# Kernel tuning notes

Measured on AMD Instinct MI355X. Metric: run time of the kernel, lower is better.

## Reference

```python
import jax, jax.numpy as jnp
import numpy as np

SHRINK_THRES = 0.0025
R_THRES = 1.0
EPS = 1e-12


def setup_inputs() -> dict:
    key = jax.random.key(0)
    k1, k2 = jax.random.split(key)
    N, L, D = 16384, 4096, 1024  # samples, memory slots (lan_dim), fea_dim
    x = jax.random.normal(k1, (N, D), dtype=jnp.float32)
    stdv = 1.0 / np.sqrt(D)
    weight = jax.random.uniform(k2, (L, D), dtype=jnp.float32, minval=-stdv, maxval=stdv)
    return {"x": x, "weight": weight}


def reference(x, weight):
    # memory addressing: att = softmax(x @ W^T)  -> [N, L]
    att = jax.nn.softmax(x @ weight.T, axis=1)
    # hard_shrink_relu: relu(a - lambd) * a / (|a - lambd| + eps)
    shifted = att - SHRINK_THRES
    att = jax.nn.relu(shifted) * att / (jnp.abs(shifted) + EPS)
    # L1 normalize along dim 1 (F.normalize p=1, eps=1e-12)
    l1 = jnp.sum(jnp.abs(att), axis=1, keepdims=True)
    att = att / jnp.maximum(l1, EPS)
    # reconstruct from memory: [N, D]
    output = att @ weight
    # nearest landmark per sample (detached gather in original)
    ind = jnp.argmax(att, axis=1)                      # [N]
    nl = weight[ind]                                   # [N, D]
    # second-nearest: overwrite argmax slot with the row minimum, re-argmax
    rows = jnp.arange(att.shape[0])
    row_min = jnp.min(att, axis=1)
    att2 = att.at[rows, ind].set(row_min)
    ind2 = jnp.argmax(att2, axis=1)
    nl2 = weight[ind2]                                 # [N, D]
    # centroid-distance filter (original returns list of indices; we return a
    # jit-compatible boolean mask over samples instead)
    cen = jnp.mean(weight, axis=0)                     # [D]
    dist = jnp.sqrt(jnp.sum((x - cen) ** 2, axis=1))   # [N]
    col_mask = dist < R_THRES                          # [N] bool
    return (output, att, nl, nl2, col_mask)
```

## Files before the change

### kernel.cpp

```cpp
#include <hip/hip_runtime.h>
#include <cmath>

#define NS 16384
#define LS 4096
#define DF 1024
#define SHRINK_T 0.0025f
#define EPS_T 1e-12f

using f16 = _Float16;
using f16x4 = __attribute__((ext_vector_type(4))) _Float16;
using f16x8 = __attribute__((ext_vector_type(8))) _Float16;
using f32x4 = __attribute__((ext_vector_type(4))) float;

__global__ void split_kernel(const float* __restrict__ src,
                             f16* __restrict__ hi, f16* __restrict__ lo, int n4) {
    int i = blockIdx.x * 256 + threadIdx.x;
    if (i >= n4) return;
    float4 v = reinterpret_cast<const float4*>(src)[i];
    f16x4 h, l;
    h[0] = (f16)v.x; h[1] = (f16)v.y; h[2] = (f16)v.z; h[3] = (f16)v.w;
    l[0] = (f16)(v.x - (float)h[0]);
    l[1] = (f16)(v.y - (float)h[1]);
    l[2] = (f16)(v.z - (float)h[2]);
    l[3] = (f16)(v.w - (float)h[3]);
    reinterpret_cast<f16x4*>(hi)[i] = h;
    reinterpret_cast<f16x4*>(lo)[i] = l;
}

__global__ void centroid_kernel(const float* __restrict__ w, float* __restrict__ cen) {
    int c = blockIdx.x * 256 + threadIdx.x;
    if (c >= DF) return;
    float acc = 0.f;
    for (int l = 0; l < LS; ++l) acc += w[(size_t)l * DF + c];
    cen[c] = acc * (1.0f / (float)LS);
}

#define BM 128
#define BN 128
#define BK 32

#define GLOAD16(gptr, lptr)                                                    \
    __builtin_amdgcn_global_load_lds(                                          \
        (const __attribute__((address_space(1))) void*)(gptr),                 \
        (__attribute__((address_space(3))) void*)(lptr), 16, 0, 0)

__global__ __launch_bounds__(256) void gemm_f16_kernel(
    const f16* __restrict__ xh, const f16* __restrict__ xl,
    const f16* __restrict__ wh, const f16* __restrict__ wl,
    float* __restrict__ S, int r0, int rowsChunk)
{
    __shared__ __align__(16) f16 Ah[BM * BK];
    __shared__ __align__(16) f16 Al[BM * BK];
    __shared__ __align__(16) f16 Bh[BN * BK];
    __shared__ __align__(16) f16 Bl[BN * BK];

    const int t = threadIdx.x;
    const int lane = t & 63;
    const int wv = t >> 6;
    const int wr = (wv >> 1) * 64;
    const int wc = (wv & 1) * 64;
    const int rowBase = r0 + blockIdx.y * BM;
    const int colBase = blockIdx.x * BN;

    f32x4 acc[4][4];
#pragma unroll
    for (int m = 0; m < 4; ++m)
#pragma unroll
        for (int n = 0; n < 4; ++n)
            acc[m][n] = (f32x4){0.f, 0.f, 0.f, 0.f};

    const int fr = lane & 15;
    const int fq = lane >> 4;
    const int kq = fq * 8;

    for (int k0 = 0; k0 < DF; k0 += BK) {
#pragma unroll
        for (int h = 0; h < 2; ++h) {
            const int sr = h * 64 + (t >> 2);
            const int cc = (t & 3) * 8;
            int ga = rowBase + sr; if (ga >= NS) ga = NS - 1;
            const int gb = colBase + sr;
            const int lbase = (h * 64 + wv * 16) * BK;
            GLOAD16(xh + (size_t)ga * DF + k0 + cc, &Ah[lbase]);
            GLOAD16(xl + (size_t)ga * DF + k0 + cc, &Al[lbase]);
            GLOAD16(wh + (size_t)gb * DF + k0 + cc, &Bh[lbase]);
            GLOAD16(wl + (size_t)gb * DF + k0 + cc, &Bl[lbase]);
        }
        __syncthreads();

        f16x8 amh[4], aml[4], bnh[4], bnl[4];
#pragma unroll
        for (int m = 0; m < 4; ++m) {
            const int r = wr + m * 16 + fr;
            amh[m] = *(const f16x8*)&Ah[r * BK + kq];
            aml[m] = *(const f16x8*)&Al[r * BK + kq];
        }
#pragma unroll
        for (int n = 0; n < 4; ++n) {
            const int c = wc + n * 16 + fr;
            bnh[n] = *(const f16x8*)&Bh[c * BK + kq];
            bnl[n] = *(const f16x8*)&Bl[c * BK + kq];
        }

#pragma unroll
        for (int m = 0; m < 4; ++m)
#pragma unroll
            for (int n = 0; n < 4; ++n) {
                acc[m][n] = __builtin_amdgcn_mfma_f32_16x16x32_f16(amh[m], bnh[n], acc[m][n], 0, 0, 0);
                acc[m][n] = __builtin_amdgcn_mfma_f32_16x16x32_f16(amh[m], bnl[n], acc[m][n], 0, 0, 0);
                acc[m][n] = __builtin_amdgcn_mfma_f32_16x16x32_f16(aml[m], bnh[n], acc[m][n], 0, 0, 0);
            }
        __syncthreads();
    }

#pragma unroll
    for (int m = 0; m < 4; ++m) {
        const int rbase = blockIdx.y * BM + wr + m * 16 + fq * 4;
#pragma unroll
        for (int n = 0; n < 4; ++n) {
            const int cc = colBase + wc + n * 16 + fr;
#pragma unroll
            for (int j = 0; j < 4; ++j) {
                const int rr = rbase + j;
                if (rr < rowsChunk)
                    S[(size_t)rr * LS + cc] = acc[m][n][j];
            }
        }
    }
}

__global__ __launch_bounds__(256) void pass2_kernel(
    const float* __restrict__ S, const float* __restrict__ x,
    const float* __restrict__ w, const float* __restrict__ cen,
    float* __restrict__ out, int r0)
{
    constexpr int T = 256;
    constexpr int PER = LS / T;
    __shared__ float att_lds[LS];
    __shared__ float red[T];
    __shared__ int redi[T];

    const int t = threadIdx.x;
    const size_t row = (size_t)r0 + blockIdx.x;
    const float* srow = S + (size_t)blockIdx.x * (size_t)LS;

    float* const out_output = out;
    float* const out_att  = out + (size_t)NS * DF;
    float* const out_nl   = out + (size_t)NS * DF + (size_t)NS * LS;
    float* const out_nl2  = out + (size_t)2 * NS * DF + (size_t)NS * LS;
    float* const out_mask = out + (size_t)3 * NS * DF + (size_t)NS * LS;

    float sv[PER];
    float mx = -INFINITY;
#pragma unroll
    for (int i = 0; i < PER; ++i) {
        sv[i] = srow[i * T + t];
        mx = fmaxf(mx, sv[i]);
    }
    red[t] = mx;
    __syncthreads();
    for (int off = 128; off >= 1; off >>= 1) {
        if (t < off) red[t] = fmaxf(red[t], red[t + off]);
        __syncthreads();
    }
    const float m = red[0];
    __syncthreads();

    float zs = 0.f;
#pragma unroll
    for (int i = 0; i < PER; ++i) {
        sv[i] = expf(sv[i] - m);
        zs += sv[i];
    }
    red[t] = zs;
    __syncthreads();
    for (int off = 128; off >= 1; off >>= 1) {
        if (t < off) red[t] += red[t + off];
        __syncthreads();
    }
    const float Z = red[0];
    __syncthreads();

    float l1 = 0.f;
#pragma unroll
    for (int i = 0; i < PER; ++i) {
        float a = sv[i] / Z;
        float r = a - SHRINK_T;
        float v = (r > 0.f) ? (r * a) / (r + EPS_T) : 0.f;
        sv[i] = v;
        l1 += v;
    }
    red[t] = l1;
    __syncthreads();
    for (int off = 128; off >= 1; off >>= 1) {
        if (t < off) red[t] += red[t + off];
        __syncthreads();
    }
    const float nrm = fmaxf(red[0], EPS_T);
    __syncthreads();

    float bv = -INFINITY; int bi = LS;
    float mn = INFINITY;
#pragma unroll
    for (int i = 0; i < PER; ++i) {
        float vn = sv[i] / nrm;
        sv[i] = vn;
        int j = i * T + t;
        att_lds[j] = vn;
        out_att[row * LS + j] = vn;
        if (vn > bv) { bv = vn; bi = j; }
        mn = fminf(mn, vn);
    }
    __syncthreads();

    red[t] = bv; redi[t] = bi;
    __syncthreads();
    for (int off = 128; off >= 1; off >>= 1) {
        if (t < off) {
            float ov = red[t + off]; int oi = redi[t + off];
            if (ov > red[t] || (ov == red[t] && oi < redi[t])) { red[t] = ov; redi[t] = oi; }
        }
        __syncthreads();
    }
    const int ind = redi[0];
    __syncthreads();

    red[t] = mn;
    __syncthreads();
    for (int off = 128; off >= 1; off >>= 1) {
        if (t < off) red[t] = fminf(red[t], red[t + off]);
        __syncthreads();
    }
    const float rowmin = red[0];
    __syncthreads();

    bv = -INFINITY; bi = LS;
#pragma unroll
    for (int i = 0; i < PER; ++i) {
        int j = i * T + t;
        float vv = (j == ind) ? rowmin : sv[i];
        if (vv > bv) { bv = vv; bi = j; }
    }
    red[t] = bv; redi[t] = bi;
    __syncthreads();
    for (int off = 128; off >= 1; off >>= 1) {
        if (t < off) {
            float ov = red[t + off]; int oi = redi[t + off];
            if (ov > red[t] || (ov == red[t] && oi < redi[t])) { red[t] = ov; redi[t] = oi; }
        }
        __syncthreads();
    }
    const int ind2 = redi[0];
    __syncthreads();

    const int lane = t & 63;
    float oa[4] = {0.f, 0.f, 0.f, 0.f};
    for (int k0 = 0; k0 < LS; k0 += 64) {
        float av = att_lds[k0 + lane];
        unsigned long long msk = __ballot(av > 0.f);
        while (msk) {
            int b = __ffsll((unsigned long long)msk) - 1;
            msk &= msk - 1;
            float vv = att_lds[k0 + b];
            const float* wr = w + (size_t)(k0 + b) * DF;
#pragma unroll
            for (int q = 0; q < 4; ++q) oa[q] = fmaf(vv, wr[t + T * q], oa[q]);
        }
    }
#pragma unroll
    for (int q = 0; q < 4; ++q)
        out_output[row * DF + t + T * q] = oa[q];

    const float* w1 = w + (size_t)ind * DF;
    const float* w2 = w + (size_t)ind2 * DF;
#pragma unroll
    for (int q = 0; q < 4; ++q) {
        out_nl[row * DF + t + T * q]  = w1[t + T * q];
        out_nl2[row * DF + t + T * q] = w2[t + T * q];
    }

    float ds = 0.f;
#pragma unroll
    for (int q = 0; q < 4; ++q) {
        float d = x[row * DF + t + T * q] - cen[t + T * q];
        ds = fmaf(d, d, ds);
    }
    red[t] = ds;
    __syncthreads();
    for (int off = 128; off >= 1; off >>= 1) {
        if (t < off) red[t] += red[t + off];
        __syncthreads();
    }
    if (t == 0) {
        float dist = sqrtf(red[0]);
        out_mask[row] = (dist < 1.0f) ? 1.0f : 0.0f;
    }
}

extern "C" void kernel_launch(void* const* d_in, const int* in_sizes, int n_in,
                              void* d_out, int out_size, void* d_ws, size_t ws_size,
                              hipStream_t stream)
{
    const float* x = (const float*)d_in[0];
    const float* w = (const float*)d_in[1];
    float* out = (float*)d_out;

    float* cen = (float*)d_ws;
    f16* xh = (f16*)(cen + DF);
    f16* xl = xh + (size_t)NS * DF;
    f16* wh = xl + (size_t)NS * DF;
    f16* wl = wh + (size_t)LS * DF;
    float* S = (float*)(wl + (size_t)LS * DF);

    const size_t head_bytes = sizeof(float) * DF + (size_t)2 * 2 * NS * DF + (size_t)2 * 2 * LS * DF;
    long cap_rows = (long)((ws_size - head_bytes) / (sizeof(float) * LS));
    if (cap_rows > NS) cap_rows = NS;
    if (cap_rows < 1) cap_rows = 1;
    int chunk = (cap_rows >= BM) ? (int)(cap_rows - (cap_rows % BM)) : (int)cap_rows;

    split_kernel<<<(NS * DF / 4 + 255) / 256, 256, 0, stream>>>(x, xh, xl, NS * DF / 4);
    split_kernel<<<(LS * DF / 4 + 255) / 256, 256, 0, stream>>>(w, wh, wl, LS * DF / 4);
    centroid_kernel<<<DF / 256, 256, 0, stream>>>(w, cen);

    for (int r0 = 0; r0 < NS; r0 += chunk) {
        int rows = (NS - r0 < chunk) ? (NS - r0) : chunk;
        dim3 grid((LS + BN - 1) / BN, (rows + BM - 1) / BM);
        gemm_f16_kernel<<<grid, 256, 0, stream>>>(xh, xl, wh, wl, S, r0, rows);
        pass2_kernel<<<rows, 256, 0, stream>>>(S, x, w, cen, out, r0);
    }
}
```

Before: 696.8 us.

## Swizzle GEMM LDS layout, parallelize centroid reduction, cap row chunk size

```diff
diff --git a/kernel.cpp b/kernel.cpp
--- a/kernel.cpp
+++ b/kernel.cpp
@@ -11,6 +11,8 @@
 using f16x4 = __attribute__((ext_vector_type(4))) _Float16;
 using f16x8 = __attribute__((ext_vector_type(8))) _Float16;
 using f32x4 = __attribute__((ext_vector_type(4))) float;
+
+#define NSEG 64
 
 __global__ void split_kernel(const float* __restrict__ src,
                              f16* __restrict__ hi, f16* __restrict__ lo, int n4) {
@@ -27,11 +29,20 @@
     reinterpret_cast<f16x4*>(lo)[i] = l;
 }
 
-__global__ void centroid_kernel(const float* __restrict__ w, float* __restrict__ cen) {
-    int c = blockIdx.x * 256 + threadIdx.x;
-    if (c >= DF) return;
+__global__ void centroid_part_kernel(const float* __restrict__ w, float* __restrict__ part) {
+    const int c = blockIdx.x * 256 + threadIdx.x;
+    const int seg = blockIdx.y;
+    const int l0 = seg * (LS / NSEG);
     float acc = 0.f;
-    for (int l = 0; l < LS; ++l) acc += w[(size_t)l * DF + c];
+    for (int l = 0; l < LS / NSEG; ++l)
+        acc += w[(size_t)(l0 + l) * DF + c];
+    part[(size_t)seg * DF + c] = acc;
+}
+
+__global__ void centroid_sum_kernel(const float* __restrict__ part, float* __restrict__ cen) {
+    const int c = blockIdx.x * 256 + threadIdx.x;
+    float acc = 0.f;
+    for (int s = 0; s < NSEG; ++s) acc += part[(size_t)s * DF + c];
     cen[c] = acc * (1.0f / (float)LS);
 }
 
@@ -43,6 +54,8 @@
     __builtin_amdgcn_global_load_lds(                                          \
         (const __attribute__((address_space(1))) void*)(gptr),                 \
         (__attribute__((address_space(3))) void*)(lptr), 16, 0, 0)
+
+__device__ __forceinline__ int swz_s(int r) { return (r & 3) ^ ((r >> 2) & 1); }
 
 __global__ __launch_bounds__(256) void gemm_f16_kernel(
     const f16* __restrict__ xh, const f16* __restrict__ xl,
@@ -71,13 +84,17 @@
 
     const int fr = lane & 15;
     const int fq = lane >> 4;
-    const int kq = fq * 8;
+
+    const int sr_lo = t >> 2;
+    const int cc_lo = ((t & 3) ^ swz_s(sr_lo)) * 8;
+    const int sr_hi = 64 + sr_lo;
+    const int cc_hi = ((t & 3) ^ swz_s(sr_hi)) * 8;
 
     for (int k0 = 0; k0 < DF; k0 += BK) {
 #pragma unroll
         for (int h = 0; h < 2; ++h) {
-            const int sr = h * 64 + (t >> 2);
-            const int cc = (t & 3) * 8;
+            const int sr = h ? sr_hi : sr_lo;
+            const int cc = h ? cc_hi : cc_lo;
             int ga = rowBase + sr; if (ga >= NS) ga = NS - 1;
             const int gb = colBase + sr;
             const int lbase = (h * 64 + wv * 16) * BK;
@@ -92,14 +109,16 @@
 #pragma unroll
         for (int m = 0; m < 4; ++m) {
             const int r = wr + m * 16 + fr;
-            amh[m] = *(const f16x8*)&Ah[r * BK + kq];
-            aml[m] = *(const f16x8*)&Al[r * BK + kq];
+            const int ca = (fq ^ swz_s(r)) * 8;
+            amh[m] = *(const f16x8*)&Ah[r * BK + ca];
+            aml[m] = *(const f16x8*)&Al[r * BK + ca];
         }
 #pragma unroll
         for (int n = 0; n < 4; ++n) {
             const int c = wc + n * 16 + fr;
-            bnh[n] = *(const f16x8*)&Bh[c * BK + kq];
-            bnl[n] = *(const f16x8*)&Bl[c * BK + kq];
+            const int cb = (fq ^ swz_s(c)) * 8;
+            bnh[n] = *(const f16x8*)&Bh[c * BK + cb];
+            bnl[n] = *(const f16x8*)&Bl[c * BK + cb];
         }
 
 #pragma unroll
@@ -306,21 +325,26 @@
     float* out = (float*)d_out;
 
     float* cen = (float*)d_ws;
-    f16* xh = (f16*)(cen + DF);
+    float* part = cen + DF;
+    f16* xh = (f16*)(part + (size_t)NSEG * DF);
     f16* xl = xh + (size_t)NS * DF;
     f16* wh = xl + (size_t)NS * DF;
     f16* wl = wh + (size_t)LS * DF;
     float* S = (float*)(wl + (size_t)LS * DF);
 
-    const size_t head_bytes = sizeof(float) * DF + (size_t)2 * 2 * NS * DF + (size_t)2 * 2 * LS * DF;
+    const size_t head_bytes = sizeof(float) * (DF + (size_t)NSEG * DF)
+                            + (size_t)2 * 2 * NS * DF + (size_t)2 * 2 * LS * DF;
     long cap_rows = (long)((ws_size - head_bytes) / (sizeof(float) * LS));
     if (cap_rows > NS) cap_rows = NS;
     if (cap_rows < 1) cap_rows = 1;
-    int chunk = (cap_rows >= BM) ? (int)(cap_rows - (cap_rows % BM)) : (int)cap_rows;
-
+    long want = 4096;
+    long pick = (cap_rows < want) ? cap_rows : want;
+    int chunk = (pick >= BM) ? (int)(pick - (pick % BM)) : (int)pick;
+
+    centroid_part_kernel<<<dim3(DF / 256, NSEG), 256, 0, stream>>>(w, part);
+    centroid_sum_kernel<<<DF / 256, 256, 0, stream>>>(part, cen);
     split_kernel<<<(NS * DF / 4 + 255) / 256, 256, 0, stream>>>(x, xh, xl, NS * DF / 4);
     split_kernel<<<(LS * DF / 4 + 255) / 256, 256, 0, stream>>>(w, wh, wl, LS * DF / 4);
-    centroid_kernel<<<DF / 256, 256, 0, stream>>>(w, cen);
 
     for (int r0 = 0; r0 < NS; r0 += chunk) {
         int rows = (NS - r0 < chunk) ? (NS - r0) : chunk;
```

Measured after the change: 703.3 us. About the same (+0.9%).
